# Kernel optimization log

Measured on AMD Instinct MI355X. Metric: run time of the kernel, lower is better.

Reference implementation:

```python
import jax, jax.numpy as jnp
import numpy as np

DIM = 768
NUM_HEADS = 12
HEAD_DIM = DIM // NUM_HEADS
SCALE = HEAD_DIM ** -0.5


def setup_inputs() -> dict:
    key = jax.random.key(0)
    ks = jax.random.split(key, 6)
    B, N, C = 4, 2048, DIM
    x = jax.random.normal(ks[0], (B, N, C), dtype=jnp.float32)
    qkv_weight = jax.random.normal(ks[1], (3 * C, C), dtype=jnp.float32) * (C ** -0.5)
    q_bias = jax.random.normal(ks[2], (C,), dtype=jnp.float32) * 0.02
    v_bias = jax.random.normal(ks[3], (C,), dtype=jnp.float32) * 0.02
    proj_weight = jax.random.normal(ks[4], (C, C), dtype=jnp.float32) * (C ** -0.5)
    proj_bias = jax.random.normal(ks[5], (C,), dtype=jnp.float32) * 0.02
    return {"x": x, "qkv_weight": qkv_weight, "q_bias": q_bias,
            "v_bias": v_bias, "proj_weight": proj_weight, "proj_bias": proj_bias}


def reference(x, qkv_weight, q_bias, v_bias, proj_weight, proj_bias):
    B, N, C = x.shape
    # bias = concat(q_bias, zeros_like(v_bias), v_bias)
    bias = jnp.concatenate([q_bias, jnp.zeros_like(v_bias), v_bias])
    qkv = x @ qkv_weight.T + bias                      # [B, N, 3C]
    qkv = qkv.reshape(B, N, 3, NUM_HEADS, HEAD_DIM)
    q, k, v = jnp.moveaxis(qkv, 2, 0)                  # each [B, N, H, hd]
    q = jnp.transpose(q, (0, 2, 1, 3)) * SCALE         # [B, H, N, hd]
    k = jnp.transpose(k, (0, 2, 1, 3))
    v = jnp.transpose(v, (0, 2, 1, 3))
    attn = jax.nn.softmax(jnp.einsum('bhqd,bhkd->bhqk', q, k), axis=-1)
    out = jnp.einsum('bhqk,bhkd->bhqd', attn, v)       # [B, H, N, hd]
    out = jnp.transpose(out, (0, 2, 1, 3)).reshape(B, N, C)
    return out @ proj_weight.T + proj_bias
```

## Files before the change

### kernel.cpp

```cpp
#include <hip/hip_runtime.h>
#include <cstdint>
#include <cstddef>

typedef _Float16 f16;
typedef _Float16 f16x8 __attribute__((ext_vector_type(8)));
typedef _Float16 f16x4 __attribute__((ext_vector_type(4)));
typedef float f32x4 __attribute__((ext_vector_type(4)));

#define DIM 768
#define NHEAD 12
#define HD 64
#define BATCH 4
#define SEQ 2048
#define MROWS (BATCH*SEQ)
#define C3 (3*DIM)
#define NBH (BATCH*NHEAD)

__device__ __forceinline__ f32x4 mfma32(f16x8 a, f16x8 b, f32x4 c) {
  return __builtin_amdgcn_mfma_f32_16x16x32_f16(a, b, c, 0, 0, 0);
}
__device__ __forceinline__ f32x4 mfma16(f16x4 a, f16x4 b, f32x4 c) {
  return __builtin_amdgcn_mfma_f32_16x16x16f16(a, b, c, 0, 0, 0);
}

__device__ __forceinline__ void gl2lds16(const void* g, void* l) {
  __builtin_amdgcn_global_load_lds(
      (const __attribute__((address_space(1))) void*)g,
      (__attribute__((address_space(3))) void*)l, 16, 0, 0);
}

__global__ __launch_bounds__(256) void k_convert(
    const float* __restrict__ x, const float* __restrict__ wqkv,
    const float* __restrict__ wproj,
    f16* __restrict__ xh, f16* __restrict__ wqh, f16* __restrict__ wph)
{
  const int NX = MROWS*DIM/4, NW = C3*DIM/4;
  int i = blockIdx.x * 256 + threadIdx.x;
  const float4* src; f16* dst; int idx;
  if (i < NX)         { src = (const float4*)x;     dst = xh;  idx = i; }
  else if (i < NX+NW) { src = (const float4*)wqkv;  dst = wqh; idx = i - NX; }
  else                { src = (const float4*)wproj; dst = wph; idx = i - NX - NW; }
  float4 v = src[idx];
  union { f16 h[4]; uint64_t u; } r;
  r.h[0] = (f16)v.x; r.h[1] = (f16)v.y; r.h[2] = (f16)v.z; r.h[3] = (f16)v.w;
  ((uint64_t*)dst)[idx] = r.u;
}

__device__ __forceinline__ void gemm_tile(
    const f16* __restrict__ A, const f16* __restrict__ B,
    int lda, int ldb, int K, int m0, int n0,
    f16* sA, f16* sB, f32x4 acc[4][4])
{
  const int tid = threadIdx.x, wid = tid >> 6;
  const int lane = tid & 63, lane15 = lane & 15, quad = lane >> 4;
  const int wm = wid >> 1, wn = wid & 1;
  for (int k0 = 0; k0 < K; k0 += 64) {
    __syncthreads();
    #pragma unroll
    for (int i = 0; i < 4; i++) {
      int j = i*256 + tid;
      int row = j >> 3;
      int sc  = (j & 7) ^ (row & 7);
      gl2lds16(A + (size_t)(m0 + row)*lda + k0 + sc*8, sA + (i*256 + wid*64)*8);
      gl2lds16(B + (size_t)(n0 + row)*ldb + k0 + sc*8, sB + (i*256 + wid*64)*8);
    }
    __syncthreads();
    #pragma unroll
    for (int ks = 0; ks < 2; ks++) {
      f16x8 af[4], bf[4];
      #pragma unroll
      for (int t = 0; t < 4; t++) {
        int ra = wm*64 + t*16 + lane15;
        af[t] = *(const f16x8*)(sA + ra*64 + (((ks*4 + quad) ^ (ra & 7)) << 3));
        int rb = wn*64 + t*16 + lane15;
        bf[t] = *(const f16x8*)(sB + rb*64 + (((ks*4 + quad) ^ (rb & 7)) << 3));
      }
      #pragma unroll
      for (int mt = 0; mt < 4; mt++)
        #pragma unroll
        for (int nt = 0; nt < 4; nt++)
          acc[mt][nt] = mfma32(af[mt], bf[nt], acc[mt][nt]);
    }
  }
}

__global__ __launch_bounds__(256, 2) void k_qkv(
    const f16* __restrict__ xh, const f16* __restrict__ wqh,
    const float* __restrict__ q_bias, const float* __restrict__ v_bias,
    f16* __restrict__ Qh, f16* __restrict__ Kh, f16* __restrict__ Vt)
{
  __shared__ f16 sA[128*64], sB[128*64];
  f32x4 acc[4][4];
  const f32x4 z4 = {0.f, 0.f, 0.f, 0.f};
  #pragma unroll
  for (int a = 0; a < 4; a++)
    #pragma unroll
    for (int b = 0; b < 4; b++) acc[a][b] = z4;

  const int m0 = blockIdx.y * 128, n0 = blockIdx.x * 128;
  gemm_tile(xh, wqh, DIM, DIM, DIM, m0, n0, sA, sB, acc);

  const int tid = threadIdx.x, wid = tid >> 6, lane = tid & 63;
  const int lane15 = lane & 15, quad = lane >> 4;
  const int wm = wid >> 1, wn = wid & 1;
  const float QS = 0.125f * 1.4426950408889634f;

  #pragma unroll
  for (int nt = 0; nt < 4; nt++) {
    int col = n0 + wn*64 + nt*16 + lane15;
    #pragma unroll
    for (int mt = 0; mt < 4; mt++) {
      #pragma unroll
      for (int r = 0; r < 4; r++) {
        int m = m0 + wm*64 + mt*16 + quad*4 + r;
        int bb = m >> 11, n = m & (SEQ - 1);
        float v = acc[mt][nt][r];
        if (n0 < DIM) {
          int h = col >> 6, d = col & 63;
          Qh[(((size_t)(bb*NHEAD + h)*SEQ + n) << 6) + d] = (f16)((v + q_bias[col]) * QS);
        } else if (n0 < 2*DIM) {
          int c2 = col - DIM; int h = c2 >> 6, d = c2 & 63;
          Kh[(((size_t)(bb*NHEAD + h)*SEQ + n) << 6) + d] = (f16)v;
        } else {
          int c2 = col - 2*DIM; int h = c2 >> 6, d = c2 & 63;
          Vt[((size_t)(bb*NHEAD + h)*HD + d)*SEQ + n] = (f16)(v + v_bias[c2]);
        }
      }
    }
  }
}

#define KVT 128
__global__ __launch_bounds__(256, 3) void k_attn(
    const f16* __restrict__ Qh, const f16* __restrict__ Kh,
    const f16* __restrict__ Vt, f16* __restrict__ attnh)
{
  __shared__ f16 sK[KVT*64];
  __shared__ f16 sV[64*KVT];

  const int tid = threadIdx.x, wid = tid >> 6, lane = tid & 63;
  const int lane15 = lane & 15, quad = lane >> 4;
  const int q0 = blockIdx.x * 128;
  const int bh = blockIdx.y;
  const int qw = q0 + wid*32;

  f16x8 qf[2][2];
  #pragma unroll
  for (int qt = 0; qt < 2; qt++)
    #pragma unroll
    for (int ks = 0; ks < 2; ks++)
      qf[qt][ks] = *(const f16x8*)(Qh + ((size_t)bh*SEQ + qw + qt*16 + lane15)*HD
                                      + ks*32 + quad*8);

  f32x4 o[4][2];
  const f32x4 z4 = {0.f, 0.f, 0.f, 0.f};
  #pragma unroll
  for (int dt = 0; dt < 4; dt++)
    #pragma unroll
    for (int qt = 0; qt < 2; qt++) o[dt][qt] = z4;
  float lI[2] = {0.f, 0.f};

  for (int kv0 = 0; kv0 < SEQ; kv0 += KVT) {
    __syncthreads();
    #pragma unroll
    for (int i = 0; i < 4; i++) {
      int j = i*256 + tid;
      int row = j >> 3;
      int sc  = (j & 7) ^ (row & 7);
      gl2lds16(Kh + ((size_t)bh*SEQ + kv0 + row)*HD + sc*8, sK + (i*256 + wid*64)*8);
    }
    #pragma unroll
    for (int i = 0; i < 4; i++) {
      int j = i*256 + tid;
      int row = j >> 4;
      int sc  = (j & 15) ^ (row & 7);
      gl2lds16(Vt + ((size_t)bh*HD + row)*SEQ + kv0 + sc*8, sV + (i*256 + wid*64)*8);
    }
    __syncthreads();

    #pragma unroll
    for (int c = 0; c < 4; c++) {
      f32x4 s[2][2];
      #pragma unroll
      for (int kt = 0; kt < 2; kt++)
        #pragma unroll
        for (int qt = 0; qt < 2; qt++) s[kt][qt] = z4;
      #pragma unroll
      for (int ks = 0; ks < 2; ks++) {
        f16x8 ka[2];
        #pragma unroll
        for (int kt = 0; kt < 2; kt++) {
          int rb = c*32 + kt*16 + lane15;
          ka[kt] = *(const f16x8*)(sK + rb*64 + (((ks*4 + quad) ^ (rb & 7)) << 3));
        }
        #pragma unroll
        for (int kt = 0; kt < 2; kt++)
          #pragma unroll
          for (int qt = 0; qt < 2; qt++)
            s[kt][qt] = mfma32(ka[kt], qf[qt][ks], s[kt][qt]);
      }
      f16x4 pb[2][2];
      #pragma unroll
      for (int kt = 0; kt < 2; kt++)
        #pragma unroll
        for (int qt = 0; qt < 2; qt++) {
          float e0 = exp2f(s[kt][qt][0]);
          float e1 = exp2f(s[kt][qt][1]);
          float e2 = exp2f(s[kt][qt][2]);
          float e3 = exp2f(s[kt][qt][3]);
          lI[qt] += (e0 + e1) + (e2 + e3);
          f16x4 p = {(f16)e0, (f16)e1, (f16)e2, (f16)e3};
          pb[kt][qt] = p;
        }
      #pragma unroll
      for (int dt = 0; dt < 4; dt++) {
        int row = dt*16 + lane15;
        #pragma unroll
        for (int kt = 0; kt < 2; kt++) {
          int c16 = 4*c + 2*kt + (quad >> 1);
          const f16* vp = sV + row*KVT + (((c16 ^ (row & 7)) << 3)) + (quad & 1)*4;
          f16x4 va = *(const f16x4*)vp;
          #pragma unroll
          for (int qt = 0; qt < 2; qt++)
            o[dt][qt] = mfma16(va, pb[kt][qt], o[dt][qt]);
        }
      }
    }
  }

  float inv[2];
  #pragma unroll
  for (int qt = 0; qt < 2; qt++) {
    float l = lI[qt];
    l += __shfl_xor(l, 16);
    l += __shfl_xor(l, 32);
    inv[qt] = 1.f / l;
  }

  __syncthreads();
  f16* tb = sK + wid * (32 * 72);
  #pragma unroll
  for (int dt = 0; dt < 4; dt++)
    #pragma unroll
    for (int qt = 0; qt < 2; qt++) {
      f32x4 v = o[dt][qt];
      float iv = inv[qt];
      f16x4 hx = {(f16)(v[0]*iv), (f16)(v[1]*iv), (f16)(v[2]*iv), (f16)(v[3]*iv)};
      *(f16x4*)(tb + (qt*16 + lane15)*72 + dt*16 + quad*4) = hx;
    }
  const int b = bh / NHEAD, h = bh % NHEAD;
  #pragma unroll
  for (int i = 0; i < 4; i++) {
    int row = i*8 + (lane >> 3);
    f16x8 rv = *(const f16x8*)(tb + row*72 + (lane & 7)*8);
    *(f16x8*)(attnh + ((size_t)b*SEQ + qw + row)*DIM + h*HD + (lane & 7)*8) = rv;
  }
}

__global__ __launch_bounds__(256, 2) void k_proj(
    const f16* __restrict__ ah, const f16* __restrict__ wph,
    const float* __restrict__ pbias, float* __restrict__ out)
{
  __shared__ f16 sA[128*64], sB[128*64];
  f32x4 acc[4][4];
  const f32x4 z4 = {0.f, 0.f, 0.f, 0.f};
  #pragma unroll
  for (int a = 0; a < 4; a++)
    #pragma unroll
    for (int b = 0; b < 4; b++) acc[a][b] = z4;

  const int m0 = blockIdx.y * 128, n0 = blockIdx.x * 128;
  gemm_tile(ah, wph, DIM, DIM, DIM, m0, n0, sA, sB, acc);

  const int tid = threadIdx.x, wid = tid >> 6, lane = tid & 63;
  const int lane15 = lane & 15, quad = lane >> 4;
  const int wm = wid >> 1, wn = wid & 1;
  #pragma unroll
  for (int nt = 0; nt < 4; nt++) {
    int col = n0 + wn*64 + nt*16 + lane15;
    float bias = pbias[col];
    #pragma unroll
    for (int mt = 0; mt < 4; mt++) {
      #pragma unroll
      for (int r = 0; r < 4; r++) {
        int m = m0 + wm*64 + mt*16 + quad*4 + r;
        out[(size_t)m*DIM + col] = acc[mt][nt][r] + bias;
      }
    }
  }
}

extern "C" void kernel_launch(void* const* d_in, const int* in_sizes, int n_in,
                              void* d_out, int out_size, void* d_ws, size_t ws_size,
                              hipStream_t stream) {
  const float* x    = (const float*)d_in[0];
  const float* wqkv = (const float*)d_in[1];
  const float* qb   = (const float*)d_in[2];
  const float* vb   = (const float*)d_in[3];
  const float* wp   = (const float*)d_in[4];
  const float* pb   = (const float*)d_in[5];
  float* out = (float*)d_out;

  f16* p = (f16*)d_ws;
  f16* xh  = p; p += (size_t)MROWS*DIM;
  f16* wqh = p; p += (size_t)C3*DIM;
  f16* wph = p; p += (size_t)DIM*DIM;
  f16* Qh  = p; p += (size_t)NBH*SEQ*HD;
  f16* Kh  = p; p += (size_t)NBH*SEQ*HD;
  f16* Vt  = p; p += (size_t)NBH*SEQ*HD;
  f16* attnh = xh;

  k_convert<<<8448, 256, 0, stream>>>(x, wqkv, wp, xh, wqh, wph);
  k_qkv<<<dim3(C3/128, MROWS/128), 256, 0, stream>>>(xh, wqh, qb, vb, Qh, Kh, Vt);
  k_attn<<<dim3(SEQ/128, NBH), 256, 0, stream>>>(Qh, Kh, Vt, attnh);
  k_proj<<<dim3(DIM/128, MROWS/128), 256, 0, stream>>>(attnh, wph, pb, out);
}
```

Before: 245.8 us.

## Stage QKV epilogue via LDS for vector stores; read K directly, MFMA row sums

The QKV GEMM epilogue now writes the tile into an LDS transpose buffer and then issues 16-byte vector stores to Q/K (row-major) and V^T, replacing scattered 2-byte global stores. In attention, K is no longer staged in LDS and is read straight from global memory into registers, leaving LDS for V only. The softmax denominator is accumulated with an MFMA against a ones vector instead of scalar adds and cross-lane shuffles. Exp results are packed with cvt_pkrtz. The QKV kernel's LDS footprint grows, which may reduce its occupancy, and the direct global K loads rely on cache hits.

```diff
diff --git a/kernel.cpp b/kernel.cpp
--- a/kernel.cpp
+++ b/kernel.cpp
@@ -5,6 +5,7 @@
 typedef _Float16 f16;
 typedef _Float16 f16x8 __attribute__((ext_vector_type(8)));
 typedef _Float16 f16x4 __attribute__((ext_vector_type(4)));
+typedef __fp16 h16x2 __attribute__((ext_vector_type(2)));
 typedef float f32x4 __attribute__((ext_vector_type(4)));
 
 #define DIM 768
@@ -90,6 +91,7 @@
     f16* __restrict__ Qh, f16* __restrict__ Kh, f16* __restrict__ Vt)
 {
   __shared__ f16 sA[128*64], sB[128*64];
+  __shared__ f16 sT[128*136];
   f32x4 acc[4][4];
   const f32x4 z4 = {0.f, 0.f, 0.f, 0.f};
   #pragma unroll
@@ -103,29 +105,61 @@
   const int tid = threadIdx.x, wid = tid >> 6, lane = tid & 63;
   const int lane15 = lane & 15, quad = lane >> 4;
   const int wm = wid >> 1, wn = wid & 1;
+  const int bb = m0 >> 11, nbase = m0 & (SEQ - 1);
   const float QS = 0.125f * 1.4426950408889634f;
 
-  #pragma unroll
-  for (int nt = 0; nt < 4; nt++) {
-    int col = n0 + wn*64 + nt*16 + lane15;
-    #pragma unroll
-    for (int mt = 0; mt < 4; mt++) {
-      #pragma unroll
-      for (int r = 0; r < 4; r++) {
-        int m = m0 + wm*64 + mt*16 + quad*4 + r;
-        int bb = m >> 11, n = m & (SEQ - 1);
-        float v = acc[mt][nt][r];
-        if (n0 < DIM) {
-          int h = col >> 6, d = col & 63;
-          Qh[(((size_t)(bb*NHEAD + h)*SEQ + n) << 6) + d] = (f16)((v + q_bias[col]) * QS);
-        } else if (n0 < 2*DIM) {
-          int c2 = col - DIM; int h = c2 >> 6, d = c2 & 63;
-          Kh[(((size_t)(bb*NHEAD + h)*SEQ + n) << 6) + d] = (f16)v;
-        } else {
-          int c2 = col - 2*DIM; int h = c2 >> 6, d = c2 & 63;
-          Vt[((size_t)(bb*NHEAD + h)*HD + d)*SEQ + n] = (f16)(v + v_bias[c2]);
+  if (n0 < 2*DIM) {
+    const bool isQ = (n0 < DIM);
+    #pragma unroll
+    for (int nt = 0; nt < 4; nt++) {
+      int col_l = wn*64 + nt*16 + lane15;
+      int col = n0 + col_l;
+      float b = isQ ? q_bias[col] : 0.f;
+      #pragma unroll
+      for (int mt = 0; mt < 4; mt++)
+        #pragma unroll
+        for (int r = 0; r < 4; r++) {
+          int m_l = wm*64 + mt*16 + quad*4 + r;
+          float v = acc[mt][nt][r] + b;
+          if (isQ) v *= QS;
+          sT[m_l*136 + col_l] = (f16)v;
         }
-      }
+    }
+    __syncthreads();
+    #pragma unroll
+    for (int it = 0; it < 8; it++) {
+      int idx = it*256 + tid;
+      int m_l = idx >> 4, ch = idx & 15;
+      f16x8 val = *(const f16x8*)(sT + m_l*136 + ch*8);
+      int col = n0 + ch*8;
+      int c2 = isQ ? col : (col - DIM);
+      int h = c2 >> 6, d = c2 & 63;
+      f16* dst = isQ ? Qh : Kh;
+      *(f16x8*)(dst + (((size_t)(bb*NHEAD + h)*SEQ + nbase + m_l) << 6) + d) = val;
+    }
+  } else {
+    #pragma unroll
+    for (int nt = 0; nt < 4; nt++) {
+      int col_l = wn*64 + nt*16 + lane15;
+      int c2 = n0 - 2*DIM + col_l;
+      float b = v_bias[c2];
+      #pragma unroll
+      for (int mt = 0; mt < 4; mt++)
+        #pragma unroll
+        for (int r = 0; r < 4; r++) {
+          int m_l = wm*64 + mt*16 + quad*4 + r;
+          sT[col_l*136 + m_l] = (f16)(acc[mt][nt][r] + b);
+        }
+    }
+    __syncthreads();
+    #pragma unroll
+    for (int it = 0; it < 8; it++) {
+      int idx = it*256 + tid;
+      int d_l = idx >> 4, m8 = idx & 15;
+      f16x8 val = *(const f16x8*)(sT + d_l*136 + m8*8);
+      int c2 = n0 - 2*DIM + d_l;
+      int h = c2 >> 6, d = c2 & 63;
+      *(f16x8*)(Vt + ((size_t)(bb*NHEAD + h)*HD + d)*SEQ + nbase + m8*8) = val;
     }
   }
 }
@@ -135,8 +169,8 @@
     const f16* __restrict__ Qh, const f16* __restrict__ Kh,
     const f16* __restrict__ Vt, f16* __restrict__ attnh)
 {
-  __shared__ f16 sK[KVT*64];
-  __shared__ f16 sV[64*KVT];
+  __shared__ f16 smem[4*32*72];
+  f16* sV = smem;
 
   const int tid = threadIdx.x, wid = tid >> 6, lane = tid & 63;
   const int lane15 = lane & 15, quad = lane >> 4;
@@ -153,22 +187,19 @@
                                       + ks*32 + quad*8);
 
   f32x4 o[4][2];
+  f32x4 sacc[2];
   const f32x4 z4 = {0.f, 0.f, 0.f, 0.f};
   #pragma unroll
   for (int dt = 0; dt < 4; dt++)
     #pragma unroll
     for (int qt = 0; qt < 2; qt++) o[dt][qt] = z4;
-  float lI[2] = {0.f, 0.f};
+  sacc[0] = z4; sacc[1] = z4;
+  const f16x4 one4 = {(f16)1.f, (f16)1.f, (f16)1.f, (f16)1.f};
+
+  const f16* Kbh = Kh + (size_t)bh*SEQ*HD;
 
   for (int kv0 = 0; kv0 < SEQ; kv0 += KVT) {
     __syncthreads();
-    #pragma unroll
-    for (int i = 0; i < 4; i++) {
-      int j = i*256 + tid;
-      int row = j >> 3;
-      int sc  = (j & 7) ^ (row & 7);
-      gl2lds16(Kh + ((size_t)bh*SEQ + kv0 + row)*HD + sc*8, sK + (i*256 + wid*64)*8);
-    }
     #pragma unroll
     for (int i = 0; i < 4; i++) {
       int j = i*256 + tid;
@@ -177,41 +208,46 @@
       gl2lds16(Vt + ((size_t)bh*HD + row)*SEQ + kv0 + sc*8, sV + (i*256 + wid*64)*8);
     }
     __syncthreads();
+    const f16* Kt = Kbh + (size_t)kv0*HD;
 
     #pragma unroll
     for (int c = 0; c < 4; c++) {
+      f16x8 ka[2][2];
+      #pragma unroll
+      for (int kt = 0; kt < 2; kt++)
+        #pragma unroll
+        for (int ks = 0; ks < 2; ks++)
+          ka[ks][kt] = *(const f16x8*)(Kt + (size_t)(c*32 + kt*16 + lane15)*HD
+                                          + ks*32 + quad*8);
       f32x4 s[2][2];
       #pragma unroll
       for (int kt = 0; kt < 2; kt++)
         #pragma unroll
         for (int qt = 0; qt < 2; qt++) s[kt][qt] = z4;
       #pragma unroll
-      for (int ks = 0; ks < 2; ks++) {
-        f16x8 ka[2];
-        #pragma unroll
-        for (int kt = 0; kt < 2; kt++) {
-          int rb = c*32 + kt*16 + lane15;
-          ka[kt] = *(const f16x8*)(sK + rb*64 + (((ks*4 + quad) ^ (rb & 7)) << 3));
-        }
+      for (int ks = 0; ks < 2; ks++)
         #pragma unroll
         for (int kt = 0; kt < 2; kt++)
           #pragma unroll
           for (int qt = 0; qt < 2; qt++)
-            s[kt][qt] = mfma32(ka[kt], qf[qt][ks], s[kt][qt]);
-      }
+            s[kt][qt] = mfma32(ka[ks][kt], qf[qt][ks], s[kt][qt]);
+
       f16x4 pb[2][2];
       #pragma unroll
       for (int kt = 0; kt < 2; kt++)
         #pragma unroll
         for (int qt = 0; qt < 2; qt++) {
-          float e0 = exp2f(s[kt][qt][0]);
-          float e1 = exp2f(s[kt][qt][1]);
-          float e2 = exp2f(s[kt][qt][2]);
-          float e3 = exp2f(s[kt][qt][3]);
-          lI[qt] += (e0 + e1) + (e2 + e3);
-          f16x4 p = {(f16)e0, (f16)e1, (f16)e2, (f16)e3};
-          pb[kt][qt] = p;
+          union { h16x2 g2[2]; f16x4 h4; } u;
+          u.g2[0] = __builtin_amdgcn_cvt_pkrtz(exp2f(s[kt][qt][0]), exp2f(s[kt][qt][1]));
+          u.g2[1] = __builtin_amdgcn_cvt_pkrtz(exp2f(s[kt][qt][2]), exp2f(s[kt][qt][3]));
+          pb[kt][qt] = u.h4;
         }
+      #pragma unroll
+      for (int kt = 0; kt < 2; kt++)
+        #pragma unroll
+        for (int qt = 0; qt < 2; qt++)
+          sacc[qt] = mfma16(one4, pb[kt][qt], sacc[qt]);
+
       #pragma unroll
       for (int dt = 0; dt < 4; dt++) {
         int row = dt*16 + lane15;
@@ -228,17 +264,10 @@
     }
   }
 
-  float inv[2];
-  #pragma unroll
-  for (int qt = 0; qt < 2; qt++) {
-    float l = lI[qt];
-    l += __shfl_xor(l, 16);
-    l += __shfl_xor(l, 32);
-    inv[qt] = 1.f / l;
-  }
+  float inv[2] = {1.f / sacc[0][0], 1.f / sacc[1][0]};
 
   __syncthreads();
-  f16* tb = sK + wid * (32 * 72);
+  f16* tb = smem + wid * (32 * 72);
   #pragma unroll
   for (int dt = 0; dt < 4; dt++)
     #pragma unroll
```

After: 254.9 us. +3.7%, slower.
